# Kernel optimization log

Measured on AMD Instinct MI355X. Metric: run time of the kernel, lower is better.

The kernel has to match this reference:

```python
import jax, jax.numpy as jnp
import numpy as np


def setup_inputs() -> dict:
    key = jax.random.key(0)
    ks = jax.random.split(key, 5)
    B, L, I, H = 512, 200, 512, 512
    x = jax.random.normal(ks[0], (B, L, I), dtype=jnp.float32)
    att = jax.random.uniform(ks[1], (L, B), dtype=jnp.float32)  # attention scores per (time, batch)
    h0 = jnp.zeros((B, H), dtype=jnp.float32)
    s = 1.0 / np.sqrt(H)
    w_ih = jax.random.uniform(ks[2], (3 * H, I), minval=-s, maxval=s, dtype=jnp.float32)
    w_hh = jax.random.uniform(ks[3], (3 * H, H), minval=-s, maxval=s, dtype=jnp.float32)
    b_ih = jnp.zeros((3 * H,), dtype=jnp.float32)
    b_hh = jnp.zeros((3 * H,), dtype=jnp.float32)
    return {"x": x, "att": att, "h0": h0, "w_ih": w_ih, "w_hh": w_hh, "b_ih": b_ih, "b_hh": b_hh}


def reference(x, att, h0, w_ih, w_hh, b_ih, b_hh):
    # x: [B,L,I] (batch_first), att: [L,B], h0: [B,H]
    # Precompute all input-hidden projections in one batched GEMM: [L,B,3H]
    gx_all = jnp.einsum('bli,gi->lbg', x, w_ih) + b_ih

    def step(h, inp):
        gx, w = inp                              # gx: [B,3H], w: [B]
        gh = h @ w_hh.T + b_hh                   # [B,3H]
        xr, xz, xn = jnp.split(gx, 3, axis=-1)
        hr, hz, hn = jnp.split(gh, 3, axis=-1)
        r = jax.nn.sigmoid(xr + hr)
        z = jax.nn.sigmoid(xz + hz)
        n = jnp.tanh(xn + r * hn)
        h_o = (1.0 - z) * n + z * h              # torch GRUCell update
        w = w[:, None]
        h_new = (1.0 - w) * h + w * h_o          # attention-weighted interpolation
        return h_new, h_new

    hx, out = jax.lax.scan(step, h0, (gx_all, att))
    out = jnp.moveaxis(out, 0, 1)  # [B,L,H] (batch_first output)
    return out, hx
```

## Files before the change

kernel.cpp:

```cpp
#include <hip/hip_runtime.h>
#include <hip/hip_fp16.h>

#define LDIM 200
#define BDIM 512
#define IDIM 512
#define HDIM 512
#define GDIM 1536
#define NGRP 16
#define NCOL 16

typedef _Float16 f16x8 __attribute__((ext_vector_type(8)));
typedef _Float16 f16x4 __attribute__((ext_vector_type(4)));
typedef float    f32x4 __attribute__((ext_vector_type(4)));

__global__ __launch_bounds__(256) void k_init(
    unsigned int* __restrict__ flags, const float* __restrict__ h0,
    _Float16* __restrict__ hb)
{
    int i = blockIdx.x * 256 + threadIdx.x;
    if (i < NGRP * NCOL) flags[i] = 0;
    if (i < BDIM * HDIM) hb[i] = (_Float16)h0[i];
}

__global__ __launch_bounds__(256) void k_pack_wfi(
    const float* __restrict__ w, f16x8* __restrict__ wf)
{
    int u = blockIdx.x * 256 + threadIdx.x;
    if (u >= (GDIM / 16) * 16 * 64) return;
    const int lane = u & 63;
    const int kk   = (u >> 6) & 15;
    const int ntg  = u >> 10;
    const int n = ntg * 16 + (lane & 15);
    const int k = kk * 32 + (lane >> 4) * 8;
    const float* src = w + (size_t)n * IDIM + k;
    f16x8 v;
    #pragma unroll
    for (int j = 0; j < 8; ++j) v[j] = (_Float16)src[j];
    wf[u] = v;
}

__global__ __launch_bounds__(256) void k_pack_wfh(
    const float* __restrict__ w, f16x8* __restrict__ wf)
{
    int u = blockIdx.x * 256 + threadIdx.x;
    if (u >= NCOL * 6 * 16 * 64) return;
    const int lane = u & 63;
    const int kk   = (u >> 6) & 15;
    const int cw   = u >> 10;
    const int wv   = cw % 6;
    const int c    = cw / 6;
    const int n_local = wv * 16 + (lane & 15);
    const int gate    = n_local >> 5;
    const int j_local = n_local & 31;
    const int n = gate * 512 + c * 32 + j_local;
    const int k = kk * 32 + (lane >> 4) * 8;
    const float* src = w + (size_t)n * HDIM + k;
    f16x8 v;
    #pragma unroll
    for (int j = 0; j < 8; ++j) v[j] = (_Float16)src[j];
    wf[u] = v;
}

__global__ __launch_bounds__(256, 2) void k_gemm_gx(
    const float* __restrict__ x, const f16x8* __restrict__ wfi,
    const float* __restrict__ bih, _Float16* __restrict__ gx)
{
    const int bid  = blockIdx.x;
    const int xcd  = bid & 7;
    const int slot = bid >> 3;
    const int gl   = slot / 3;
    const int ng   = slot % 3;
    const int m0   = (xcd * 200 + gl) * 64;
    const int n0   = ng * 512;

    const int t   = threadIdx.x;
    const int wid = t >> 6;
    const int l   = t & 63;

    __shared__ __align__(16) _Float16 As[64 * 512];

    {
        const int r  = t >> 2;
        const int k0 = (t & 3) * 128;
        const int m  = m0 + r;
        const float* src = x + ((size_t)(m & 511) * LDIM + (m >> 9)) * IDIM + k0;
        #pragma unroll
        for (int jj = 0; jj < 16; ++jj) {
            const float4 v0 = *(const float4*)(src + jj * 8);
            const float4 v1 = *(const float4*)(src + jj * 8 + 4);
            f16x8 hq;
            hq[0] = (_Float16)v0.x; hq[1] = (_Float16)v0.y;
            hq[2] = (_Float16)v0.z; hq[3] = (_Float16)v0.w;
            hq[4] = (_Float16)v1.x; hq[5] = (_Float16)v1.y;
            hq[6] = (_Float16)v1.z; hq[7] = (_Float16)v1.w;
            const int byte = (r * 1024 + (k0 + jj * 8) * 2) ^ ((r & 7) << 4);
            *(f16x8*)((char*)As + byte) = hq;
        }
    }
    __syncthreads();

    const f16x8* bp = wfi + (size_t)((ng * 4 + wid) * 8) * 1024 + l;
    const int kb8   = (l >> 4) * 16;
    const int rbase = l & 15;

    f32x4 acc[4][8] = {};

    for (int kk = 0; kk < 16; ++kk) {
        f16x8 a[4];
        #pragma unroll
        for (int mt = 0; mt < 4; ++mt) {
            const int r = mt * 16 + rbase;
            const int byte = (r * 1024 + kk * 64 + kb8) ^ ((r & 7) << 4);
            a[mt] = *(const f16x8*)((const char*)As + byte);
        }
        const f16x8* bk = bp + kk * 64;
        #pragma unroll
        for (int nt = 0; nt < 8; ++nt) {
            const f16x8 bf = bk[(size_t)nt * 1024];
            #pragma unroll
            for (int mt = 0; mt < 4; ++mt)
                acc[mt][nt] = __builtin_amdgcn_mfma_f32_16x16x32_f16(a[mt], bf, acc[mt][nt], 0, 0, 0);
        }
    }

    #pragma unroll
    for (int nt = 0; nt < 8; ++nt) {
        const int n = n0 + wid * 128 + nt * 16 + (l & 15);
        const float bv = bih[n];
        #pragma unroll
        for (int mt = 0; mt < 4; ++mt) {
            #pragma unroll
            for (int r = 0; r < 4; ++r) {
                const int m = m0 + mt * 16 + (l >> 4) * 4 + r;
                gx[(size_t)m * GDIM + n] = (_Float16)(acc[mt][nt][r] + bv);
            }
        }
    }
}

__global__ __launch_bounds__(384) void k_recur(
    const _Float16* __restrict__ gx, const float* __restrict__ att,
    const float* __restrict__ h0, const f16x8* __restrict__ wfh,
    const float* __restrict__ bhh, _Float16* __restrict__ hb,
    unsigned int* __restrict__ flags, float* __restrict__ out,
    float* __restrict__ hx)
{
    const int bid = blockIdx.x;
    const int g = bid >> 4;
    const int c = bid & 15;
    const int t = threadIdx.x;
    const int w = t >> 6;
    const int l = t & 63;

    __shared__ __align__(16) _Float16 h16[32 * 512];
    __shared__ float ghsT[32][100];

    f16x8 B[16];
    {
        const f16x8* p = wfh + (size_t)(c * 6 + w) * 1024 + l;
        #pragma unroll
        for (int kk = 0; kk < 16; ++kk) B[kk] = p[kk * 64];
    }

    const int i  = t >> 3;
    const int j4 = (t & 7) * 4;

    float bhr[4], bhz[4], bhn[4], hv[4];
    if (t < 256) {
        const float4 r4 = *(const float4*)(bhh + c * 32 + j4);
        const float4 z4 = *(const float4*)(bhh + 512 + c * 32 + j4);
        const float4 n4 = *(const float4*)(bhh + 1024 + c * 32 + j4);
        bhr[0]=r4.x; bhr[1]=r4.y; bhr[2]=r4.z; bhr[3]=r4.w;
        bhz[0]=z4.x; bhz[1]=z4.y; bhz[2]=z4.z; bhz[3]=z4.w;
        bhn[0]=n4.x; bhn[1]=n4.y; bhn[2]=n4.z; bhn[3]=n4.w;
        const float4 h4 = *(const float4*)(h0 + (size_t)(g * 32 + i) * 512 + c * 32 + j4);
        hv[0]=h4.x; hv[1]=h4.y; hv[2]=h4.z; hv[3]=h4.w;
    }

    const unsigned int* fline = flags + g * 16;
    unsigned int* myflag = flags + g * 16 + c;

    const int ib = (l >> 4) * 4;
    const int nl = w * 16 + (l & 15);
    const int k8 = (l >> 4) * 8;
    const int rr0 = l & 15;
    const int rr1 = rr0 + 16;

    f16x4 cr = {}, cz = {}, cn = {};
    float ca = 0.f;
    if (t < 256) {
        const _Float16* gp = gx + ((size_t)(g * 32 + i)) * GDIM + c * 32 + j4;
        cr = *(const f16x4*)(gp);
        cz = *(const f16x4*)(gp + 512);
        cn = *(const f16x4*)(gp + 1024);
        ca = att[g * 32 + i];
    }

    int rd = 0;
    for (int s = 0; s < LDIM; ++s) {
        if (s > 0 && w == 0) {
            const unsigned int* fp = fline + (l & 15);
            unsigned int fv;
            do {
                asm volatile("global_load_dword %0, %1, off sc0 sc1\n\t"
                             "s_waitcnt vmcnt(0)"
                             : "=v"(fv) : "v"(fp) : "memory");
            } while (fv < (unsigned int)s);
        }
        __syncthreads();

        if (t < 256) {
            const unsigned long long* hsrc = (const unsigned long long*)
                (hb + (size_t)rd * (BDIM * HDIM) + (size_t)g * 32 * 512);
            unsigned long long vv[16];
            #pragma unroll
            for (int q = 0; q < 16; ++q) {
                asm volatile("global_load_dwordx2 %0, %1, off sc0 sc1"
                             : "=v"(vv[q]) : "v"(hsrc + q * 256 + t));
            }
            asm volatile("s_waitcnt vmcnt(0)" ::: "memory");
            __builtin_amdgcn_sched_barrier(0);
            #pragma unroll
            for (int q = 0; q < 16; ++q) {
                const int idx = q * 256 + t;
                const int row = idx >> 7;
                const int c8  = idx & 127;
                const int byte = (row * 1024 + c8 * 8) ^ ((row & 7) << 4);
                *(unsigned long long*)((char*)h16 + byte) = vv[q];
            }
        }

        f16x4 nr = {}, nz = {}, nn2 = {};
        float na = 0.f;
        if (t < 256) {
            const int sn = (s < LDIM - 1) ? s + 1 : s;
            const _Float16* gp = gx + ((size_t)sn * BDIM + g * 32 + i) * GDIM + c * 32 + j4;
            nr  = *(const f16x4*)(gp);
            nz  = *(const f16x4*)(gp + 512);
            nn2 = *(const f16x4*)(gp + 1024);
            na  = att[(size_t)sn * BDIM + g * 32 + i];
        }
        __syncthreads();

        f32x4 acc0 = {0.f, 0.f, 0.f, 0.f};
        f32x4 acc1 = {0.f, 0.f, 0.f, 0.f};
        #pragma unroll
        for (int kk = 0; kk < 16; ++kk) {
            const int kb = kk * 64 + k8 * 2;
            const int b0 = (rr0 * 1024 + kb) ^ ((rr0 & 7) << 4);
            const int b1 = (rr1 * 1024 + kb) ^ ((rr1 & 7) << 4);
            const f16x8 a0 = *(const f16x8*)((const char*)h16 + b0);
            const f16x8 a1 = *(const f16x8*)((const char*)h16 + b1);
            acc0 = __builtin_amdgcn_mfma_f32_16x16x32_f16(a0, B[kk], acc0, 0, 0, 0);
            acc1 = __builtin_amdgcn_mfma_f32_16x16x32_f16(a1, B[kk], acc1, 0, 0, 0);
        }
        #pragma unroll
        for (int q = 0; q < 4; ++q) {
            ghsT[ib + q][nl]      = acc0[q];
            ghsT[16 + ib + q][nl] = acc1[q];
        }
        __syncthreads();

        const int wr = (rd == 2) ? 0 : rd + 1;
        float o[4];
        if (t < 256) {
            const float4 ghr = *(const float4*)&ghsT[i][j4];
            const float4 ghz = *(const float4*)&ghsT[i][32 + j4];
            const float4 ghn = *(const float4*)&ghsT[i][64 + j4];
            const float hrr[4] = {ghr.x, ghr.y, ghr.z, ghr.w};
            const float hzz[4] = {ghz.x, ghz.y, ghz.z, ghz.w};
            const float hnn[4] = {ghn.x, ghn.y, ghn.z, ghn.w};
            f16x4 hp;
            #pragma unroll
            for (int q = 0; q < 4; ++q) {
                const float hr = hrr[q] + bhr[q];
                const float hz = hzz[q] + bhz[q];
                const float hn = hnn[q] + bhn[q];
                const float h  = hv[q];
                const float rg = 1.f / (1.f + __expf(-((float)cr[q] + hr)));
                const float zg = 1.f / (1.f + __expf(-((float)cz[q] + hz)));
                const float ng = tanhf((float)cn[q] + rg * hn);
                const float ho = (1.f - zg) * ng + zg * h;
                const float hnew = (1.f - ca) * h + ca * ho;
                hv[q] = hnew;
                o[q] = hnew;
                hp[q] = (_Float16)hnew;
            }
            union { f16x4 v; unsigned long long u; } pk; pk.v = hp;
            _Float16* hd = hb + (size_t)wr * (BDIM * HDIM)
                         + (size_t)(g * 32 + i) * 512 + c * 32 + j4;
            asm volatile("global_store_dwordx2 %0, %1, off sc0 sc1"
                         :: "v"(hd), "v"(pk.u) : "memory");
            asm volatile("s_waitcnt vmcnt(0)" ::: "memory");
        }
        __syncthreads();
        if (t == 0) {
            unsigned int fv = (unsigned int)(s + 1);
            asm volatile("global_store_dword %0, %1, off sc0 sc1"
                         :: "v"(myflag), "v"(fv) : "memory");
        }
        if (t < 256) {
            *(float4*)(out + ((size_t)(g * 32 + i) * LDIM + s) * HDIM + c * 32 + j4)
                = *(float4*)o;
        }
        cr = nr; cz = nz; cn = nn2; ca = na;
        rd = wr;
    }

    if (t < 256) {
        float o[4] = {hv[0], hv[1], hv[2], hv[3]};
        *(float4*)(hx + (size_t)(g * 32 + i) * 512 + c * 32 + j4) = *(float4*)o;
    }
}

extern "C" void kernel_launch(void* const* d_in, const int* in_sizes, int n_in,
                              void* d_out, int out_size, void* d_ws, size_t ws_size,
                              hipStream_t stream)
{
    const float* x   = (const float*)d_in[0];
    const float* att = (const float*)d_in[1];
    const float* h0  = (const float*)d_in[2];
    const float* wih = (const float*)d_in[3];
    const float* whh = (const float*)d_in[4];
    const float* bih = (const float*)d_in[5];
    const float* bhh = (const float*)d_in[6];

    float* out = (float*)d_out;
    float* hx  = out + (size_t)BDIM * LDIM * HDIM;

    char* ws = (char*)d_ws;
    f16x8*        wfA   = (f16x8*)ws;
    unsigned int* flags = (unsigned int*)(ws + 0x180000);
    _Float16*     hb    = (_Float16*)(ws + 0x190000);
    _Float16*     gx    = (_Float16*)(ws + 0x310000);

    k_init<<<1024, 256, 0, stream>>>(flags, h0, hb);
    k_pack_wfi<<<384, 256, 0, stream>>>(wih, wfA);
    k_gemm_gx<<<4800, 256, 0, stream>>>(x, wfA, bih, gx);
    k_pack_wfh<<<384, 256, 0, stream>>>(whh, wfA);
    k_recur<<<256, 384, 0, stream>>>(gx, att, h0, wfA, bhh, hb, flags, out, hx);
}
```

Before: 1.360 ms.

## Replace flag-based inter-block sync with step tags embedded in hidden-state data

Each hidden-state chunk is now stored as a 16-byte record holding four fp16 values plus the step number. Readers poll the data itself until every tag matches the current step, instead of spinning on a separate per-group flag array. This drops the store-wait, the extra barrier and the separate flag store and poll round trips on the critical path of each timestep. In exchange, each state exchange moves twice as many bytes, and every reader thread may re-issue its 16 loads while other blocks are still catching up.

```diff
diff --git a/kernel.cpp b/kernel.cpp
--- a/kernel.cpp
+++ b/kernel.cpp
@@ -12,14 +12,20 @@
 typedef _Float16 f16x8 __attribute__((ext_vector_type(8)));
 typedef _Float16 f16x4 __attribute__((ext_vector_type(4)));
 typedef float    f32x4 __attribute__((ext_vector_type(4)));
+typedef unsigned int u32x4 __attribute__((ext_vector_type(4)));
 
 __global__ __launch_bounds__(256) void k_init(
-    unsigned int* __restrict__ flags, const float* __restrict__ h0,
-    _Float16* __restrict__ hb)
-{
-    int i = blockIdx.x * 256 + threadIdx.x;
-    if (i < NGRP * NCOL) flags[i] = 0;
-    if (i < BDIM * HDIM) hb[i] = (_Float16)h0[i];
+    const float* __restrict__ h0, u32x4* __restrict__ hb2)
+{
+    int u = blockIdx.x * 256 + threadIdx.x;
+    if (u >= BDIM * HDIM / 4) return;
+    const int row = u >> 7, col4 = u & 127;
+    const float4 v = *(const float4*)(h0 + (size_t)row * HDIM + col4 * 4);
+    union { f16x4 h; unsigned int d[2]; } pk;
+    pk.h[0] = (_Float16)v.x; pk.h[1] = (_Float16)v.y;
+    pk.h[2] = (_Float16)v.z; pk.h[3] = (_Float16)v.w;
+    u32x4 st; st[0] = pk.d[0]; st[1] = pk.d[1]; st[2] = 0u; st[3] = 0u;
+    hb2[u] = st;
 }
 
 __global__ __launch_bounds__(256) void k_pack_wfi(
@@ -141,9 +147,8 @@
 __global__ __launch_bounds__(384) void k_recur(
     const _Float16* __restrict__ gx, const float* __restrict__ att,
     const float* __restrict__ h0, const f16x8* __restrict__ wfh,
-    const float* __restrict__ bhh, _Float16* __restrict__ hb,
-    unsigned int* __restrict__ flags, float* __restrict__ out,
-    float* __restrict__ hx)
+    const float* __restrict__ bhh, char* __restrict__ hb2c,
+    float* __restrict__ out, float* __restrict__ hx)
 {
     const int bid = blockIdx.x;
     const int g = bid >> 4;
@@ -177,9 +182,6 @@
         hv[0]=h4.x; hv[1]=h4.y; hv[2]=h4.z; hv[3]=h4.w;
     }
 
-    const unsigned int* fline = flags + g * 16;
-    unsigned int* myflag = flags + g * 16 + c;
-
     const int ib = (l >> 4) * 4;
     const int nl = w * 16 + (l & 15);
     const int k8 = (l >> 4) * 8;
@@ -198,27 +200,22 @@
 
     int rd = 0;
     for (int s = 0; s < LDIM; ++s) {
-        if (s > 0 && w == 0) {
-            const unsigned int* fp = fline + (l & 15);
-            unsigned int fv;
-            do {
-                asm volatile("global_load_dword %0, %1, off sc0 sc1\n\t"
-                             "s_waitcnt vmcnt(0)"
-                             : "=v"(fv) : "v"(fp) : "memory");
-            } while (fv < (unsigned int)s);
-        }
-        __syncthreads();
-
+        u32x4 vv[16];
         if (t < 256) {
-            const unsigned long long* hsrc = (const unsigned long long*)
-                (hb + (size_t)rd * (BDIM * HDIM) + (size_t)g * 32 * 512);
-            unsigned long long vv[16];
-            #pragma unroll
-            for (int q = 0; q < 16; ++q) {
-                asm volatile("global_load_dwordx2 %0, %1, off sc0 sc1"
-                             : "=v"(vv[q]) : "v"(hsrc + q * 256 + t));
+            const char* hbase = hb2c
+                + ((size_t)rd * 65536 + (size_t)g * 4096 + t) * 16;
+            bool again = true;
+            while (again) {
+                #pragma unroll
+                for (int q = 0; q < 16; ++q)
+                    asm volatile("global_load_dwordx4 %0, %1, off sc0 sc1"
+                                 : "=v"(vv[q]) : "v"(hbase + (size_t)q * 4096));
+                asm volatile("s_waitcnt vmcnt(0)" ::: "memory");
+                again = false;
+                #pragma unroll
+                for (int q = 0; q < 16; ++q)
+                    again |= (vv[q][2] != (unsigned)s);
             }
-            asm volatile("s_waitcnt vmcnt(0)" ::: "memory");
             __builtin_amdgcn_sched_barrier(0);
             #pragma unroll
             for (int q = 0; q < 16; ++q) {
@@ -226,7 +223,9 @@
                 const int row = idx >> 7;
                 const int c8  = idx & 127;
                 const int byte = (row * 1024 + c8 * 8) ^ ((row & 7) << 4);
-                *(unsigned long long*)((char*)h16 + byte) = vv[q];
+                union { unsigned int d[2]; unsigned long long u; } m;
+                m.d[0] = vv[q][0]; m.d[1] = vv[q][1];
+                *(unsigned long long*)((char*)h16 + byte) = m.u;
             }
         }
 
@@ -262,7 +261,6 @@
         __syncthreads();
 
         const int wr = (rd == 2) ? 0 : rd + 1;
-        float o[4];
         if (t < 256) {
             const float4 ghr = *(const float4*)&ghsT[i][j4];
             const float4 ghz = *(const float4*)&ghsT[i][32 + j4];
@@ -270,6 +268,7 @@
             const float hrr[4] = {ghr.x, ghr.y, ghr.z, ghr.w};
             const float hzz[4] = {ghz.x, ghz.y, ghz.z, ghz.w};
             const float hnn[4] = {ghn.x, ghn.y, ghn.z, ghn.w};
+            float o[4];
             f16x4 hp;
             #pragma unroll
             for (int q = 0; q < 4; ++q) {
@@ -286,20 +285,14 @@
                 o[q] = hnew;
                 hp[q] = (_Float16)hnew;
             }
-            union { f16x4 v; unsigned long long u; } pk; pk.v = hp;
-            _Float16* hd = hb + (size_t)wr * (BDIM * HDIM)
-                         + (size_t)(g * 32 + i) * 512 + c * 32 + j4;
-            asm volatile("global_store_dwordx2 %0, %1, off sc0 sc1"
-                         :: "v"(hd), "v"(pk.u) : "memory");
-            asm volatile("s_waitcnt vmcnt(0)" ::: "memory");
-        }
-        __syncthreads();
-        if (t == 0) {
-            unsigned int fv = (unsigned int)(s + 1);
-            asm volatile("global_store_dword %0, %1, off sc0 sc1"
-                         :: "v"(myflag), "v"(fv) : "memory");
-        }
-        if (t < 256) {
+            union { f16x4 v; unsigned int d[2]; } pk; pk.v = hp;
+            u32x4 st;
+            st[0] = pk.d[0]; st[1] = pk.d[1];
+            st[2] = (unsigned)(s + 1); st[3] = (unsigned)(s + 1);
+            char* hd = hb2c + ((size_t)wr * 65536
+                     + (size_t)(g * 32 + i) * 128 + (size_t)c * 8 + (t & 7)) * 16;
+            asm volatile("global_store_dwordx4 %0, %1, off sc0 sc1"
+                         :: "v"(hd), "v"(st) : "memory");
             *(float4*)(out + ((size_t)(g * 32 + i) * LDIM + s) * HDIM + c * 32 + j4)
                 = *(float4*)o;
         }
@@ -329,14 +322,13 @@
     float* hx  = out + (size_t)BDIM * LDIM * HDIM;
 
     char* ws = (char*)d_ws;
-    f16x8*        wfA   = (f16x8*)ws;
-    unsigned int* flags = (unsigned int*)(ws + 0x180000);
-    _Float16*     hb    = (_Float16*)(ws + 0x190000);
-    _Float16*     gx    = (_Float16*)(ws + 0x310000);
-
-    k_init<<<1024, 256, 0, stream>>>(flags, h0, hb);
+    f16x8*    wfA = (f16x8*)ws;
+    char*     hb2 = ws + 0x180000;
+    _Float16* gx  = (_Float16*)(ws + 0x480000);
+
+    k_init<<<256, 256, 0, stream>>>(h0, (u32x4*)hb2);
     k_pack_wfi<<<384, 256, 0, stream>>>(wih, wfA);
     k_gemm_gx<<<4800, 256, 0, stream>>>(x, wfA, bih, gx);
     k_pack_wfh<<<384, 256, 0, stream>>>(whh, wfA);
-    k_recur<<<256, 384, 0, stream>>>(gx, att, h0, wfA, bhh, hb, flags, out, hx);
-}
+    k_recur<<<256, 384, 0, stream>>>(gx, att, h0, wfA, bhh, hb2, out, hx);
+}
```

After: 1.359 ms. No clear change (-0.1%).
